# Kernel optimization log

Hardware: AMD Instinct MI355X
Metric: run time of the kernel (lower is better)

## Reference

```python
import jax, jax.numpy as jnp
import numpy as np

TABLE = 4194304   # maxGridFeatId[-1]
D = 4             # eachGridFeatDim
L = 6             # gridFeatLevelCnt (code indexes sigma1..sigma6)
DIR = 16          # in_dim_dir
H = 64            # hidden_dim_color
B, N = 16384, 128


def _linear_init(key, fan_in, fan_out):
    # matches torch nn.Linear default U(-1/sqrt(fan_in), 1/sqrt(fan_in))
    s = 1.0 / np.sqrt(fan_in)
    kw, kb = jax.random.split(key)
    W = jax.random.uniform(kw, (fan_in, fan_out), minval=-s, maxval=s, dtype=jnp.float32)
    b = jax.random.uniform(kb, (fan_out,), minval=-s, maxval=s, dtype=jnp.float32)
    return W, b


def setup_inputs() -> dict:
    key = jax.random.key(0)
    ks = jax.random.split(key, 6)
    x = jax.random.randint(ks[0], (B, N, L), 0, TABLE)
    d = jax.random.normal(ks[1], (B, DIR), dtype=jnp.float32)
    gridWeight = jax.random.uniform(ks[2], (TABLE, D), dtype=jnp.float32)  # torch.rand
    in0 = DIR + L * (D - 1)  # 16 + 18 = 34
    W0, b0 = _linear_init(ks[3], in0, H)
    W1, b1 = _linear_init(ks[4], H, H)
    W2, b2 = _linear_init(ks[5], H, 3)
    return dict(x=x, d=d, gridWeight=gridWeight, W0=W0, b0=b0, W1=W1, b1=b1, W2=W2, b2=b2)


def reference(x, d, gridWeight, W0, b0, W1, b1, W2, b2):
    Bv, Nv, Lv = x.shape
    Dv = gridWeight.shape[-1]
    # embedding gather: (B, N, L, D); same memory order as torch reshape(B, N*L, D)
    feat = gridWeight[x]
    # per-level densities, clipped then multiplied (prod over the 6 levels)
    sig = jnp.clip(feat[..., 0], 0.0, 1.0)                 # (B, N, L)
    sigma0 = jnp.prod(sig, axis=-1, keepdims=True) + 1e-4  # (B, N, 1)
    sigma = sigma0 / jnp.max(sigma0, axis=1, keepdims=True)
    # geometric features: (B, N, L*(D-1))
    geo = feat[..., 1:].reshape(Bv, Nv, Lv * (Dv - 1))
    h = jnp.concatenate([jnp.broadcast_to(d[:, None, :], (Bv, Nv, d.shape[-1])), geo], axis=-1)
    h = jax.nn.relu(h @ W0 + b0)
    h = jax.nn.relu(h @ W1 + b1)
    color = jax.nn.sigmoid(h @ W2 + b2)                    # (B, N, 3)
    # alpha compositing: NOTE original does torch.cumprod(..., dim=2) on a
    # (B, N, 1) tensor, i.e. cumprod over a size-1 axis == identity. Faithful.
    alpha = 1.0 - sigma
    transparentBefore = jnp.concatenate(
        [jnp.ones((Bv, 1, 1), dtype=sigma.dtype), alpha[:, :-1]], axis=1)
    colorWeight0 = transparentBefore * sigma               # (B, N, 1)
    colorOut = colorWeight0 * color                        # (B, N, 3)
    return sigma, jnp.sum(colorOut, axis=1)                # (B,N,1), (B,3)
```

## Files before the change

kernel.cpp:

```cpp
#include <hip/hip_runtime.h>
#include <hip/hip_bf16.h>
#include <math.h>


typedef short bf16x8 __attribute__((ext_vector_type(8)));
typedef float floatx4 __attribute__((ext_vector_type(4)));

__device__ inline unsigned short f2b(float f) {
    union { float f; unsigned u; } v; v.f = f;
    unsigned r = v.u + 0x7FFF + ((v.u >> 16) & 1);
    return (unsigned short)(r >> 16);
}
__device__ inline unsigned pk2(float a, float b) {
    return (unsigned)f2b(a) | ((unsigned)f2b(b) << 16);
}

__global__ void build_frags(const float* __restrict__ W0,
                            const float* __restrict__ W1,
                            const float* __restrict__ W2,
                            unsigned short* __restrict__ wsf) {
    int tid = blockIdx.x * blockDim.x + threadIdx.x;
    if (tid >= 7168) return;
    int lane, j, k, n;
    float val;
    if (tid < 2048) {
        int f = tid >> 9, r = tid & 511; lane = r >> 3; j = r & 7;
        k = ((lane >> 4) * 8) + j;
        n = f * 16 + (lane & 15);
        val = (k < 18) ? W0[(16 + k) * 64 + n] : 0.0f;
    } else if (tid < 6144) {
        int e = tid - 2048;
        int f = e >> 9, r = e & 511; lane = r >> 3; j = r & 7;
        int ks = f >> 2, nt = f & 3;
        k = ks * 32 + ((lane >> 4) * 8) + j;
        n = nt * 16 + (lane & 15);
        val = W1[k * 64 + n];
    } else {
        int e = tid - 6144;
        int f = e >> 9, r = e & 511; lane = r >> 3; j = r & 7;
        k = f * 32 + ((lane >> 4) * 8) + j;
        n = lane & 15;
        val = (n < 3) ? W2[k * 3 + n] : 0.0f;
    }
    wsf[tid] = f2b(val);
}

__global__ __launch_bounds__(256) void surf_main(
    const int*   __restrict__ x,
    const float* __restrict__ dvec,
    const float* __restrict__ gw,
    const float* __restrict__ W0,
    const float* __restrict__ b0v,
    const float* __restrict__ b1v,
    const float* __restrict__ b2v,
    const unsigned short* __restrict__ wsf,
    float* __restrict__ out_sigma,
    float* __restrict__ out_color)
{
    const int t    = threadIdx.x;
    const int lane = t & 63;
    const int w    = t >> 6;
    const int l15  = lane & 15;
    const int quad = lane >> 4;
    const size_t ray = (size_t)blockIdx.x * 4 + w;

    __shared__ unsigned short A0[4][128 * 40];
    __shared__ unsigned short HT[4][16 * 72];
    __shared__ float cwL[4][128];
    __shared__ float dwL[4][64];

    unsigned short* A0w = A0[w];
    unsigned short* HTw = HT[w];
    float* cww = cwL[w];
    float* dww = dwL[w];

    const int* xp = x + ray * 768 + lane * 12;
    const int4 xa = *(const int4*)(xp);
    const int4 xb = *(const int4*)(xp + 4);
    const int4 xc = *(const int4*)(xp + 8);

    float4 g[12];
    g[0]  = *(const float4*)(gw + (size_t)xa.x * 4);
    g[1]  = *(const float4*)(gw + (size_t)xa.y * 4);
    g[2]  = *(const float4*)(gw + (size_t)xa.z * 4);
    g[3]  = *(const float4*)(gw + (size_t)xa.w * 4);
    g[4]  = *(const float4*)(gw + (size_t)xb.x * 4);
    g[5]  = *(const float4*)(gw + (size_t)xb.y * 4);
    g[6]  = *(const float4*)(gw + (size_t)xb.z * 4);
    g[7]  = *(const float4*)(gw + (size_t)xb.w * 4);
    g[8]  = *(const float4*)(gw + (size_t)xc.x * 4);
    g[9]  = *(const float4*)(gw + (size_t)xc.y * 4);
    g[10] = *(const float4*)(gw + (size_t)xc.z * 4);
    g[11] = *(const float4*)(gw + (size_t)xc.w * 4);

    {
        float acc = b0v[lane];
        const float* db = dvec + ray * 16;
        #pragma unroll
        for (int i = 0; i < 16; ++i) acc = fmaf(db[i], W0[i * 64 + lane], acc);
        dww[lane] = acc;
    }

    float sig0[2];
    #pragma unroll
    for (int p = 0; p < 2; ++p) {
        const float4* gp = g + 6 * p;
        float s = 1.0f;
        #pragma unroll
        for (int l = 0; l < 6; ++l)
            s *= fminf(fmaxf(gp[l].x, 0.0f), 1.0f);
        sig0[p] = s + 1e-4f;
        unsigned u0 = pk2(gp[0].y, gp[0].z);
        unsigned u1 = pk2(gp[0].w, gp[1].y);
        unsigned u2 = pk2(gp[1].z, gp[1].w);
        unsigned u3 = pk2(gp[2].y, gp[2].z);
        unsigned u4 = pk2(gp[2].w, gp[3].y);
        unsigned u5 = pk2(gp[3].z, gp[3].w);
        unsigned u6 = pk2(gp[4].y, gp[4].z);
        unsigned u7 = pk2(gp[4].w, gp[5].y);
        unsigned u8 = pk2(gp[5].z, gp[5].w);
        int4* dst = (int4*)(A0w + (lane * 2 + p) * 40);
        dst[0] = make_int4((int)u0, (int)u1, (int)u2, (int)u3);
        dst[1] = make_int4((int)u4, (int)u5, (int)u6, (int)u7);
        dst[2] = make_int4((int)u8, 0, 0, 0);
        dst[3] = make_int4(0, 0, 0, 0);
    }

    float m = fmaxf(sig0[0], sig0[1]);
    #pragma unroll
    for (int off = 1; off < 64; off <<= 1)
        m = fmaxf(m, __shfl_xor(m, off));
    const float sp0 = sig0[0] / m;
    const float sp1 = sig0[1] / m;
    {
        float2 sv; sv.x = sp0; sv.y = sp1;
        *(float2*)(out_sigma + ray * 128 + lane * 2) = sv;
    }
    const float prev = __shfl_up(sp1, 1);
    const float cw0 = (lane == 0) ? sp0 : (1.0f - prev) * sp0;
    const float cw1 = (1.0f - sp0) * sp1;
    {
        float2 cv; cv.x = cw0; cv.y = cw1;
        *(float2*)(cww + lane * 2) = cv;
    }

    bf16x8 bw0[4], bw1[8], bw2[2];
    #pragma unroll
    for (int i = 0; i < 4; ++i) bw0[i] = *(const bf16x8*)(wsf + i * 512 + lane * 8);
    #pragma unroll
    for (int i = 0; i < 8; ++i) bw1[i] = *(const bf16x8*)(wsf + 2048 + i * 512 + lane * 8);
    bw2[0] = *(const bf16x8*)(wsf + 6144 + lane * 8);
    bw2[1] = *(const bf16x8*)(wsf + 6656 + lane * 8);
    float b1r[4];
    #pragma unroll
    for (int nt = 0; nt < 4; ++nt) b1r[nt] = b1v[nt * 16 + l15];
    const float b2r = (l15 < 3) ? b2v[l15] : 0.0f;
    float dw4[4];
    #pragma unroll
    for (int nt = 0; nt < 4; ++nt) dw4[nt] = dww[nt * 16 + l15];

    float csum = 0.0f;
    for (int mt = 0; mt < 8; ++mt) {
        bf16x8 a0 = *(const bf16x8*)(A0w + (mt * 16 + l15) * 40 + quad * 8);

        floatx4 acc0[4];
        #pragma unroll
        for (int nt = 0; nt < 4; ++nt) {
            float dw = dw4[nt];
            acc0[nt] = (floatx4){dw, dw, dw, dw};
            acc0[nt] = __builtin_amdgcn_mfma_f32_16x16x32_bf16(a0, bw0[nt], acc0[nt], 0, 0, 0);
        }
        #pragma unroll
        for (int nt = 0; nt < 4; ++nt)
            #pragma unroll
            for (int r = 0; r < 4; ++r)
                HTw[(quad * 4 + r) * 72 + nt * 16 + l15] = f2b(fmaxf(acc0[nt][r], 0.0f));

        bf16x8 a1a = *(const bf16x8*)(HTw + l15 * 72 + quad * 8);
        bf16x8 a1b = *(const bf16x8*)(HTw + l15 * 72 + 32 + quad * 8);
        floatx4 acc1[4];
        #pragma unroll
        for (int nt = 0; nt < 4; ++nt) {
            float bb = b1r[nt];
            acc1[nt] = (floatx4){bb, bb, bb, bb};
            acc1[nt] = __builtin_amdgcn_mfma_f32_16x16x32_bf16(a1a, bw1[nt],     acc1[nt], 0, 0, 0);
            acc1[nt] = __builtin_amdgcn_mfma_f32_16x16x32_bf16(a1b, bw1[4 + nt], acc1[nt], 0, 0, 0);
        }
        #pragma unroll
        for (int nt = 0; nt < 4; ++nt)
            #pragma unroll
            for (int r = 0; r < 4; ++r)
                HTw[(quad * 4 + r) * 72 + nt * 16 + l15] = f2b(fmaxf(acc1[nt][r], 0.0f));

        bf16x8 a2a = *(const bf16x8*)(HTw + l15 * 72 + quad * 8);
        bf16x8 a2b = *(const bf16x8*)(HTw + l15 * 72 + 32 + quad * 8);
        floatx4 acc2 = (floatx4){b2r, b2r, b2r, b2r};
        acc2 = __builtin_amdgcn_mfma_f32_16x16x32_bf16(a2a, bw2[0], acc2, 0, 0, 0);
        acc2 = __builtin_amdgcn_mfma_f32_16x16x32_bf16(a2b, bw2[1], acc2, 0, 0, 0);

        floatx4 cwq = *(const floatx4*)(cww + mt * 16 + quad * 4);
        #pragma unroll
        for (int r = 0; r < 4; ++r)
            csum += cwq[r] / (1.0f + __expf(-acc2[r]));
    }

    csum += __shfl_xor(csum, 16);
    csum += __shfl_xor(csum, 32);
    if (lane < 3) out_color[ray * 3 + lane] = csum;
}

extern "C" void kernel_launch(void* const* d_in, const int* in_sizes, int n_in,
                              void* d_out, int out_size, void* d_ws, size_t ws_size,
                              hipStream_t stream) {
    const int*   x    = (const int*)d_in[0];
    const float* dvec = (const float*)d_in[1];
    const float* gw   = (const float*)d_in[2];
    const float* W0   = (const float*)d_in[3];
    const float* b0   = (const float*)d_in[4];
    const float* W1   = (const float*)d_in[5];
    const float* b1   = (const float*)d_in[6];
    const float* W2   = (const float*)d_in[7];
    const float* b2   = (const float*)d_in[8];

    const int B = in_sizes[1] / 16;
    float* out_sigma = (float*)d_out;
    float* out_color = (float*)d_out + (size_t)B * 128;
    unsigned short* wsf = (unsigned short*)d_ws;

    build_frags<<<14, 512, 0, stream>>>(W0, W1, W2, wsf);
    surf_main<<<B / 4, 256, 0, stream>>>(x, dvec, gw, W0, b0, b1, b2, wsf,
                                         out_sigma, out_color);
}
```

Before: 349.7 us.

## Fold weight fragment build into main kernel and shrink A0 shared staging

Removes the separate build_frags launch: each wave now loads W0/W1/W2 directly from global memory and packs them into bf16 MFMA fragments in registers. The A0 shared buffer shrinks from 40 to 24 shorts per row, with the ninth packed pair kept in a separate array and the zero padding built in registers, which cuts LDS use so more blocks can be resident (launch_bounds now asks for 4). Weight loads and the direction projection are moved ahead of the gather loads. In exchange, every wave does many scalar strided weight loads and bf16 conversions, which is redundant work repeated per block.

Result: slower. 379.4 us (+8.5%).

```diff
diff --git a/kernel.cpp b/kernel.cpp
--- a/kernel.cpp
+++ b/kernel.cpp
@@ -14,46 +14,22 @@
 __device__ inline unsigned pk2(float a, float b) {
     return (unsigned)f2b(a) | ((unsigned)f2b(b) << 16);
 }
-
-__global__ void build_frags(const float* __restrict__ W0,
-                            const float* __restrict__ W1,
-                            const float* __restrict__ W2,
-                            unsigned short* __restrict__ wsf) {
-    int tid = blockIdx.x * blockDim.x + threadIdx.x;
-    if (tid >= 7168) return;
-    int lane, j, k, n;
-    float val;
-    if (tid < 2048) {
-        int f = tid >> 9, r = tid & 511; lane = r >> 3; j = r & 7;
-        k = ((lane >> 4) * 8) + j;
-        n = f * 16 + (lane & 15);
-        val = (k < 18) ? W0[(16 + k) * 64 + n] : 0.0f;
-    } else if (tid < 6144) {
-        int e = tid - 2048;
-        int f = e >> 9, r = e & 511; lane = r >> 3; j = r & 7;
-        int ks = f >> 2, nt = f & 3;
-        k = ks * 32 + ((lane >> 4) * 8) + j;
-        n = nt * 16 + (lane & 15);
-        val = W1[k * 64 + n];
-    } else {
-        int e = tid - 6144;
-        int f = e >> 9, r = e & 511; lane = r >> 3; j = r & 7;
-        k = f * 32 + ((lane >> 4) * 8) + j;
-        n = lane & 15;
-        val = (n < 3) ? W2[k * 3 + n] : 0.0f;
-    }
-    wsf[tid] = f2b(val);
-}
-
-__global__ __launch_bounds__(256) void surf_main(
+__device__ inline bf16x8 frag_from(unsigned a, unsigned b, unsigned c, unsigned d) {
+    union { unsigned u[4]; bf16x8 v; } t;
+    t.u[0] = a; t.u[1] = b; t.u[2] = c; t.u[3] = d;
+    return t.v;
+}
+
+__global__ __launch_bounds__(256, 4) void surf_main(
     const int*   __restrict__ x,
     const float* __restrict__ dvec,
     const float* __restrict__ gw,
     const float* __restrict__ W0,
     const float* __restrict__ b0v,
+    const float* __restrict__ W1,
     const float* __restrict__ b1v,
+    const float* __restrict__ W2,
     const float* __restrict__ b2v,
-    const unsigned short* __restrict__ wsf,
     float* __restrict__ out_sigma,
     float* __restrict__ out_color)
 {
@@ -64,12 +40,14 @@
     const int quad = lane >> 4;
     const size_t ray = (size_t)blockIdx.x * 4 + w;
 
-    __shared__ unsigned short A0[4][128 * 40];
+    __shared__ unsigned short A0[4][128 * 24];
+    __shared__ unsigned int   G67[4][128];
     __shared__ unsigned short HT[4][16 * 72];
     __shared__ float cwL[4][128];
     __shared__ float dwL[4][64];
 
     unsigned short* A0w = A0[w];
+    unsigned int*   G67w = G67[w];
     unsigned short* HTw = HT[w];
     float* cww = cwL[w];
     float* dww = dwL[w];
@@ -78,6 +56,56 @@
     const int4 xa = *(const int4*)(xp);
     const int4 xb = *(const int4*)(xp + 4);
     const int4 xc = *(const int4*)(xp + 8);
+
+    const int kq = quad * 8;
+    bf16x8 bw0[4], bw1[8], bw2[2];
+    #pragma unroll
+    for (int nt = 0; nt < 4; ++nt) {
+        const int n = nt * 16 + l15;
+        unsigned fr[4];
+        #pragma unroll
+        for (int jj = 0; jj < 4; ++jj) {
+            const int k0 = kq + 2 * jj, k1 = k0 + 1;
+            const float f0 = (k0 < 18) ? W0[(16 + k0) * 64 + n] : 0.0f;
+            const float f1 = (k1 < 18) ? W0[(16 + k1) * 64 + n] : 0.0f;
+            fr[jj] = pk2(f0, f1);
+        }
+        bw0[nt] = frag_from(fr[0], fr[1], fr[2], fr[3]);
+    }
+    #pragma unroll
+    for (int i = 0; i < 8; ++i) {
+        const int kb = (i >> 2) * 32 + kq;
+        const int n  = (i & 3) * 16 + l15;
+        unsigned fr[4];
+        #pragma unroll
+        for (int jj = 0; jj < 4; ++jj)
+            fr[jj] = pk2(W1[(kb + 2 * jj) * 64 + n], W1[(kb + 2 * jj + 1) * 64 + n]);
+        bw1[i] = frag_from(fr[0], fr[1], fr[2], fr[3]);
+    }
+    #pragma unroll
+    for (int s = 0; s < 2; ++s) {
+        const int kb = s * 32 + kq;
+        unsigned fr[4];
+        #pragma unroll
+        for (int jj = 0; jj < 4; ++jj) {
+            const float f0 = (l15 < 3) ? W2[(kb + 2 * jj) * 3 + l15] : 0.0f;
+            const float f1 = (l15 < 3) ? W2[(kb + 2 * jj + 1) * 3 + l15] : 0.0f;
+            fr[jj] = pk2(f0, f1);
+        }
+        bw2[s] = frag_from(fr[0], fr[1], fr[2], fr[3]);
+    }
+    float b1r[4];
+    #pragma unroll
+    for (int nt = 0; nt < 4; ++nt) b1r[nt] = b1v[nt * 16 + l15];
+    const float b2r = (l15 < 3) ? b2v[l15] : 0.0f;
+
+    {
+        float acc = b0v[lane];
+        const float* db = dvec + ray * 16;
+        #pragma unroll
+        for (int i = 0; i < 16; ++i) acc = fmaf(db[i], W0[i * 64 + lane], acc);
+        dww[lane] = acc;
+    }
 
     float4 g[12];
     g[0]  = *(const float4*)(gw + (size_t)xa.x * 4);
@@ -93,14 +121,6 @@
     g[10] = *(const float4*)(gw + (size_t)xc.z * 4);
     g[11] = *(const float4*)(gw + (size_t)xc.w * 4);
 
-    {
-        float acc = b0v[lane];
-        const float* db = dvec + ray * 16;
-        #pragma unroll
-        for (int i = 0; i < 16; ++i) acc = fmaf(db[i], W0[i * 64 + lane], acc);
-        dww[lane] = acc;
-    }
-
     float sig0[2];
     #pragma unroll
     for (int p = 0; p < 2; ++p) {
@@ -110,20 +130,20 @@
         for (int l = 0; l < 6; ++l)
             s *= fminf(fmaxf(gp[l].x, 0.0f), 1.0f);
         sig0[p] = s + 1e-4f;
-        unsigned u0 = pk2(gp[0].y, gp[0].z);
-        unsigned u1 = pk2(gp[0].w, gp[1].y);
-        unsigned u2 = pk2(gp[1].z, gp[1].w);
-        unsigned u3 = pk2(gp[2].y, gp[2].z);
-        unsigned u4 = pk2(gp[2].w, gp[3].y);
-        unsigned u5 = pk2(gp[3].z, gp[3].w);
-        unsigned u6 = pk2(gp[4].y, gp[4].z);
-        unsigned u7 = pk2(gp[4].w, gp[5].y);
-        unsigned u8 = pk2(gp[5].z, gp[5].w);
-        int4* dst = (int4*)(A0w + (lane * 2 + p) * 40);
+        const unsigned u0 = pk2(gp[0].y, gp[0].z);
+        const unsigned u1 = pk2(gp[0].w, gp[1].y);
+        const unsigned u2 = pk2(gp[1].z, gp[1].w);
+        const unsigned u3 = pk2(gp[2].y, gp[2].z);
+        const unsigned u4 = pk2(gp[2].w, gp[3].y);
+        const unsigned u5 = pk2(gp[3].z, gp[3].w);
+        const unsigned u6 = pk2(gp[4].y, gp[4].z);
+        const unsigned u7 = pk2(gp[4].w, gp[5].y);
+        const unsigned u8 = pk2(gp[5].z, gp[5].w);
+        const int pt = lane * 2 + p;
+        int4* dst = (int4*)(A0w + pt * 24);
         dst[0] = make_int4((int)u0, (int)u1, (int)u2, (int)u3);
         dst[1] = make_int4((int)u4, (int)u5, (int)u6, (int)u7);
-        dst[2] = make_int4((int)u8, 0, 0, 0);
-        dst[3] = make_int4(0, 0, 0, 0);
+        G67w[pt] = u8;
     }
 
     float m = fmaxf(sig0[0], sig0[1]);
@@ -144,29 +164,27 @@
         *(float2*)(cww + lane * 2) = cv;
     }
 
-    bf16x8 bw0[4], bw1[8], bw2[2];
-    #pragma unroll
-    for (int i = 0; i < 4; ++i) bw0[i] = *(const bf16x8*)(wsf + i * 512 + lane * 8);
-    #pragma unroll
-    for (int i = 0; i < 8; ++i) bw1[i] = *(const bf16x8*)(wsf + 2048 + i * 512 + lane * 8);
-    bw2[0] = *(const bf16x8*)(wsf + 6144 + lane * 8);
-    bw2[1] = *(const bf16x8*)(wsf + 6656 + lane * 8);
-    float b1r[4];
-    #pragma unroll
-    for (int nt = 0; nt < 4; ++nt) b1r[nt] = b1v[nt * 16 + l15];
-    const float b2r = (l15 < 3) ? b2v[l15] : 0.0f;
     float dw4[4];
     #pragma unroll
     for (int nt = 0; nt < 4; ++nt) dw4[nt] = dww[nt * 16 + l15];
+
+    const bool qlt2 = (quad < 2);
+    const bool q2   = (quad == 2);
 
     float csum = 0.0f;
     for (int mt = 0; mt < 8; ++mt) {
-        bf16x8 a0 = *(const bf16x8*)(A0w + (mt * 16 + l15) * 40 + quad * 8);
+        const int row = mt * 16 + l15;
+        const int4 av = *(const int4*)(A0w + row * 24 + (quad & 1) * 8);
+        const unsigned gv = G67w[row];
+        bf16x8 a0 = frag_from(qlt2 ? (unsigned)av.x : (q2 ? gv : 0u),
+                              qlt2 ? (unsigned)av.y : 0u,
+                              qlt2 ? (unsigned)av.z : 0u,
+                              qlt2 ? (unsigned)av.w : 0u);
 
         floatx4 acc0[4];
         #pragma unroll
         for (int nt = 0; nt < 4; ++nt) {
-            float dw = dw4[nt];
+            const float dw = dw4[nt];
             acc0[nt] = (floatx4){dw, dw, dw, dw};
             acc0[nt] = __builtin_amdgcn_mfma_f32_16x16x32_bf16(a0, bw0[nt], acc0[nt], 0, 0, 0);
         }
@@ -181,7 +199,7 @@
         floatx4 acc1[4];
         #pragma unroll
         for (int nt = 0; nt < 4; ++nt) {
-            float bb = b1r[nt];
+            const float bb = b1r[nt];
             acc1[nt] = (floatx4){bb, bb, bb, bb};
             acc1[nt] = __builtin_amdgcn_mfma_f32_16x16x32_bf16(a1a, bw1[nt],     acc1[nt], 0, 0, 0);
             acc1[nt] = __builtin_amdgcn_mfma_f32_16x16x32_bf16(a1b, bw1[4 + nt], acc1[nt], 0, 0, 0);
@@ -198,7 +216,7 @@
         acc2 = __builtin_amdgcn_mfma_f32_16x16x32_bf16(a2a, bw2[0], acc2, 0, 0, 0);
         acc2 = __builtin_amdgcn_mfma_f32_16x16x32_bf16(a2b, bw2[1], acc2, 0, 0, 0);
 
-        floatx4 cwq = *(const floatx4*)(cww + mt * 16 + quad * 4);
+        const floatx4 cwq = *(const floatx4*)(cww + mt * 16 + quad * 4);
         #pragma unroll
         for (int r = 0; r < 4; ++r)
             csum += cwq[r] / (1.0f + __expf(-acc2[r]));
@@ -225,9 +243,7 @@
     const int B = in_sizes[1] / 16;
     float* out_sigma = (float*)d_out;
     float* out_color = (float*)d_out + (size_t)B * 128;
-    unsigned short* wsf = (unsigned short*)d_ws;
-
-    build_frags<<<14, 512, 0, stream>>>(W0, W1, W2, wsf);
-    surf_main<<<B / 4, 256, 0, stream>>>(x, dvec, gw, W0, b0, b1, b2, wsf,
+
+    surf_main<<<B / 4, 256, 0, stream>>>(x, dvec, gw, W0, b0, W1, b1, W2, b2,
                                          out_sigma, out_color);
 }
```
